# Kernel optimization log

Hardware: AMD Instinct MI355X
Metric: run time of the kernel (lower is better)

The kernel has to match this reference:

```python
import jax, jax.numpy as jnp
import numpy as np

E, K = 32, 8              # num_experts, top_k
H, I = 2048, 768          # hidden_size, moe_intermediate_size
B, S = 1, 1024            # batch, seq_len


def setup_inputs() -> dict:
    key = jax.random.key(0)
    k0, k1, k2, k3, k4 = jax.random.split(key, 5)
    scale = 0.02
    return {
        "hidden_states": jax.random.normal(k0, (B, S, H), jnp.float32),
        "gate_w":        jax.random.normal(k1, (E, H), jnp.float32) * scale,   # router, nn.Linear(H->E) weight
        "gate_proj_w":   jax.random.normal(k2, (E, I, H), jnp.float32) * scale,
        "up_proj_w":     jax.random.normal(k3, (E, I, H), jnp.float32) * scale,
        "down_proj_w":   jax.random.normal(k4, (E, H, I), jnp.float32) * scale,
    }


def reference(hidden_states, gate_w, gate_proj_w, up_proj_w, down_proj_w):
    b, s, h = hidden_states.shape
    flat = hidden_states.reshape(-1, h)                     # [T, H]
    T = flat.shape[0]

    # router
    router_logits = flat @ gate_w.T                          # [T, E]
    probs = jax.nn.softmax(router_logits.astype(jnp.float32), axis=-1)
    top_w, top_i = jax.lax.top_k(probs, K)                   # [T, K]
    top_w = top_w / jnp.sum(top_w, axis=-1, keepdims=True)   # norm_topk_prob=True
    top_w = top_w.astype(flat.dtype)

    # dense combine weights: zero for unselected experts -> same math as
    # the per-expert gather/scatter loop in the torch reference
    combine = jnp.zeros((T, E), flat.dtype).at[
        jnp.arange(T)[:, None], top_i].add(top_w)            # [T, E]

    # SwiGLU expert MLPs, batched over experts
    g = jnp.einsum('th,eih->eti', flat, gate_proj_w)         # [E, T, I]
    u = jnp.einsum('th,eih->eti', flat, up_proj_w)           # [E, T, I]
    act = jax.nn.silu(g) * u                                 # [E, T, I]
    out_e = jnp.einsum('eti,ehi->eth', act, down_proj_w)     # [E, T, H]

    final = jnp.einsum('eth,te->th', out_e, combine)         # [T, H]
    return final.reshape(b, s, h), router_logits
```

## Files before the change

### kernel.cpp

```cpp
#include <hip/hip_runtime.h>

typedef __attribute__((ext_vector_type(8))) short short8;
typedef __attribute__((ext_vector_type(8))) unsigned short ushort8;
typedef __attribute__((ext_vector_type(4))) float floatx4;

#define T_TOK 1024
#define H_DIM 2048
#define I_DIM 768
#define E_NUM 32
#define TOPK  8

#define OFF_CNT   0
#define OFF_OFFS  512
#define OFF_LIST  1024
#define OFF_TIDX  132096
#define OFF_TPOS  164864
#define OFF_TW    197632
#define OFF_ACT   262144
#define OFF_XG    12845056
#define OFF_Y     OFF_XG

__device__ __forceinline__ unsigned short f2bf(float f) {
  unsigned int u = __builtin_bit_cast(unsigned int, f);
  u += 0x7fffu + ((u >> 16) & 1u);
  return (unsigned short)(u >> 16);
}
__device__ __forceinline__ float bf2f(unsigned short h) {
  unsigned int u = ((unsigned int)h) << 16;
  return __builtin_bit_cast(float, u);
}
__device__ __forceinline__ void async_copy16(const void* g, void* l) {
  __builtin_amdgcn_global_load_lds(
      (const __attribute__((address_space(1))) unsigned int*)g,
      (__attribute__((address_space(3))) unsigned int*)l, 16, 0, 0);
}

__global__ __launch_bounds__(256) void router_kernel(
    const float* __restrict__ x, const float* __restrict__ gw,
    float* __restrict__ logits_out, int* __restrict__ cnt, int* __restrict__ list,
    int* __restrict__ tidx, int* __restrict__ tpos, float* __restrict__ tw)
{
  int t = blockIdx.x;
  int tid = threadIdx.x;
  int wave = tid >> 6, lane = tid & 63;
  const float* xr = x + (size_t)t * H_DIM;
  float xv[32];
#pragma unroll
  for (int i = 0; i < 32; i++) xv[i] = xr[lane + 64 * i];

  __shared__ float lg[E_NUM];
  for (int ee = 0; ee < 8; ee++) {
    int e = wave * 8 + ee;
    const float* wr = gw + (size_t)e * H_DIM;
    float acc = 0.f;
#pragma unroll
    for (int i = 0; i < 32; i++) acc += xv[i] * wr[lane + 64 * i];
    for (int m = 32; m >= 1; m >>= 1) acc += __shfl_xor(acc, m, 64);
    if (lane == 0) lg[e] = acc;
  }
  __syncthreads();

  if (tid < E_NUM) logits_out[t * E_NUM + tid] = lg[tid];

  if (wave == 0) {
    float logit = (lane < E_NUM) ? lg[lane] : -1e30f;
    float mx = logit;
    for (int m = 16; m >= 1; m >>= 1) mx = fmaxf(mx, __shfl_xor(mx, m, 64));
    float p = (lane < E_NUM) ? expf(logit - mx) : 0.f;
    float sum = p;
    for (int m = 16; m >= 1; m >>= 1) sum += __shfl_xor(sum, m, 64);
    p /= sum;

    float rem = (lane < E_NUM) ? p : -1.f;
    int   seli[TOPK];
    float selw[TOPK];
    float sumw = 0.f;
#pragma unroll
    for (int k = 0; k < TOPK; k++) {
      float v = rem; int i = lane;
      for (int m = 16; m >= 1; m >>= 1) {
        float ov = __shfl_xor(v, m, 64);
        int   oi = __shfl_xor(i, m, 64);
        if (ov > v || (ov == v && oi < i)) { v = ov; i = oi; }
      }
      seli[k] = i; selw[k] = v; sumw += v;
      if (lane == i) rem = -1.f;
    }
    if (lane < TOPK) {
      int e = seli[lane];
      float w = selw[lane] / sumw;
      int pos = atomicAdd(&cnt[e], 1);
      list[e * 1024 + pos] = t;
      tidx[t * TOPK + lane] = e;
      tpos[t * TOPK + lane] = pos;
      tw[t * TOPK + lane] = w;
    }
  }
}

__global__ void scan_kernel(const int* __restrict__ cnt, int* __restrict__ offs) {
  if (threadIdx.x == 0) {
    int s = 0;
    for (int e = 0; e < E_NUM; e++) { offs[e] = s; s += cnt[e]; }
    offs[E_NUM] = s;
  }
}

__global__ __launch_bounds__(256) void gather_x(
    const float* __restrict__ x, const int* __restrict__ tidx,
    const int* __restrict__ tpos, const int* __restrict__ offs,
    unsigned short* __restrict__ xg)
{
  int t = blockIdx.x;
  int tid = threadIdx.x;
  const float* xr = x + (size_t)t * H_DIM + tid * 8;
  floatx4 a = *(const floatx4*)xr;
  floatx4 b = *(const floatx4*)(xr + 4);
  ushort8 p;
#pragma unroll
  for (int j = 0; j < 4; j++) { p[j] = f2bf(a[j]); p[j + 4] = f2bf(b[j]); }
#pragma unroll
  for (int k = 0; k < TOPK; k++) {
    int e = tidx[t * TOPK + k];
    int slot = offs[e] + tpos[t * TOPK + k];
    *(ushort8*)(xg + (size_t)slot * H_DIM + tid * 8) = p;
  }
}

__global__ __launch_bounds__(256, 2) void gemm_gu(
    const unsigned short* __restrict__ xg,
    const float* __restrict__ gpw, const float* __restrict__ upw,
    const int* __restrict__ cnt, const int* __restrict__ offs,
    unsigned short* __restrict__ act)
{
  int bid = blockIdx.x;
  int e = bid & 31;
  int nt = bid >> 5;
  int c = cnt[e];
  if (c == 0) return;
  int base = offs[e];
  int n0 = nt * 32;

  __shared__ unsigned char  As[512 * 64];
  __shared__ unsigned short Ws[64 * 40];

  int tid = threadIdx.x;
  int w = tid >> 6, lane = tid & 63;
  int q = lane >> 4, l15 = lane & 15;

  int wr = tid >> 2, wc = tid & 3;
  const float* wp = (wr < 32 ? gpw + ((size_t)e * I_DIM + n0 + wr) * H_DIM
                             : upw + ((size_t)e * I_DIM + n0 + (wr - 32)) * H_DIM) + wc * 8;
  unsigned short* wdst = &Ws[wr * 40 + wc * 8];

  const unsigned short* agp[8];
  unsigned char* aldst[8];
  {
    int rl = lane >> 2;
    int ch = (lane & 3) ^ ((lane >> 3) & 3);
#pragma unroll
    for (int g = 0; g < 8; g++) {
      int rm = w * 128 + g * 16 + rl;
      int slot = base + rm; if (slot > 8191) slot = 8191;
      agp[g] = xg + (size_t)slot * H_DIM + ch * 8;
      aldst[g] = &As[(w * 128 + g * 16) * 64];
    }
  }
  const unsigned char* afp[8];
#pragma unroll
  for (int i = 0; i < 8; i++) {
    int row = w * 128 + i * 16 + l15;
    int chunk = q ^ ((row >> 1) & 3);
    afp[i] = &As[row * 64 + chunk * 16];
  }
  const unsigned short* bfp[4];
#pragma unroll
  for (int j = 0; j < 4; j++) bfp[j] = &Ws[(j * 16 + l15) * 40 + q * 8];

  int rem = c - w * 128;
  int ni = rem <= 0 ? 0 : (rem >= 128 ? 8 : ((rem + 15) >> 4));
  bool wact = ni > 0;

  floatx4 acc[8][4];
#pragma unroll
  for (int i = 0; i < 8; i++)
#pragma unroll
    for (int j = 0; j < 4; j++) acc[i][j] = (floatx4){0.f, 0.f, 0.f, 0.f};

  for (int kt = 0; kt < H_DIM / 32; kt++) {
    if (wact) {
#pragma unroll
      for (int g = 0; g < 8; g++) { async_copy16(agp[g], aldst[g]); agp[g] += 32; }
    }
    floatx4 w0 = *(const floatx4*)wp;
    floatx4 w1 = *(const floatx4*)(wp + 4);
    wp += 32;
    ushort8 pw;
#pragma unroll
    for (int z = 0; z < 4; z++) { pw[z] = f2bf(w0[z]); pw[z + 4] = f2bf(w1[z]); }
    *(ushort8*)wdst = pw;
    __syncthreads();

    short8 bf[4];
#pragma unroll
    for (int j = 0; j < 4; j++) bf[j] = *(const short8*)bfp[j];
#pragma unroll
    for (int i = 0; i < 8; i++) {
      if (i < ni) {
        short8 af = *(const short8*)afp[i];
#pragma unroll
        for (int j = 0; j < 4; j++)
          acc[i][j] = __builtin_amdgcn_mfma_f32_16x16x32_bf16(af, bf[j], acc[i][j], 0, 0, 0);
      }
    }
    __syncthreads();
  }

#pragma unroll
  for (int i = 0; i < 8; i++) {
    if (i < ni) {
#pragma unroll
      for (int r = 0; r < 4; r++) {
        int s = w * 128 + i * 16 + q * 4 + r;
        if (s < c) {
          size_t rowb = (size_t)(base + s) * I_DIM + n0;
#pragma unroll
          for (int j = 0; j < 2; j++) {
            float g = acc[i][j][r];
            float u = acc[i][j + 2][r];
            float sv = g / (1.f + __expf(-g));
            act[rowb + j * 16 + l15] = f2bf(sv * u);
          }
        }
      }
    }
  }
}

__global__ __launch_bounds__(256, 2) void gemm_down(
    const unsigned short* __restrict__ act,
    const float* __restrict__ dpw,
    const int* __restrict__ cnt, const int* __restrict__ offs,
    unsigned short* __restrict__ y)
{
  int bid = blockIdx.x;
  int e = bid & 31;
  int nt = bid >> 5;
  int c = cnt[e];
  if (c == 0) return;
  int base = offs[e];
  int h0 = nt * 64;

  __shared__ unsigned char  As[512 * 64];
  __shared__ unsigned short Ws[64 * 40];

  int tid = threadIdx.x;
  int w = tid >> 6, lane = tid & 63;
  int q = lane >> 4, l15 = lane & 15;

  int wr = tid >> 2, wc = tid & 3;
  const float* wp = dpw + ((size_t)e * H_DIM + h0 + wr) * I_DIM + wc * 8;
  unsigned short* wdst = &Ws[wr * 40 + wc * 8];

  const unsigned short* agp[8];
  unsigned char* aldst[8];
  {
    int rl = lane >> 2;
    int ch = (lane & 3) ^ ((lane >> 3) & 3);
#pragma unroll
    for (int g = 0; g < 8; g++) {
      int rm = w * 128 + g * 16 + rl;
      int slot = base + rm; if (slot > 8191) slot = 8191;
      agp[g] = act + (size_t)slot * I_DIM + ch * 8;
      aldst[g] = &As[(w * 128 + g * 16) * 64];
    }
  }
  const unsigned char* afp[8];
#pragma unroll
  for (int i = 0; i < 8; i++) {
    int row = w * 128 + i * 16 + l15;
    int chunk = q ^ ((row >> 1) & 3);
    afp[i] = &As[row * 64 + chunk * 16];
  }
  const unsigned short* bfp[4];
#pragma unroll
  for (int j = 0; j < 4; j++) bfp[j] = &Ws[(j * 16 + l15) * 40 + q * 8];

  int rem = c - w * 128;
  int ni = rem <= 0 ? 0 : (rem >= 128 ? 8 : ((rem + 15) >> 4));
  bool wact = ni > 0;

  floatx4 acc[8][4];
#pragma unroll
  for (int i = 0; i < 8; i++)
#pragma unroll
    for (int j = 0; j < 4; j++) acc[i][j] = (floatx4){0.f, 0.f, 0.f, 0.f};

  for (int kt = 0; kt < I_DIM / 32; kt++) {
    if (wact) {
#pragma unroll
      for (int g = 0; g < 8; g++) { async_copy16(agp[g], aldst[g]); agp[g] += 32; }
    }
    floatx4 w0 = *(const floatx4*)wp;
    floatx4 w1 = *(const floatx4*)(wp + 4);
    wp += 32;
    ushort8 pw;
#pragma unroll
    for (int z = 0; z < 4; z++) { pw[z] = f2bf(w0[z]); pw[z + 4] = f2bf(w1[z]); }
    *(ushort8*)wdst = pw;
    __syncthreads();

    short8 bf[4];
#pragma unroll
    for (int j = 0; j < 4; j++) bf[j] = *(const short8*)bfp[j];
#pragma unroll
    for (int i = 0; i < 8; i++) {
      if (i < ni) {
        short8 af = *(const short8*)afp[i];
#pragma unroll
        for (int j = 0; j < 4; j++)
          acc[i][j] = __builtin_amdgcn_mfma_f32_16x16x32_bf16(af, bf[j], acc[i][j], 0, 0, 0);
      }
    }
    __syncthreads();
  }

#pragma unroll
  for (int i = 0; i < 8; i++) {
    if (i < ni) {
#pragma unroll
      for (int r = 0; r < 4; r++) {
        int s = w * 128 + i * 16 + q * 4 + r;
        if (s < c) {
          size_t rowb = (size_t)(base + s) * H_DIM + h0;
#pragma unroll
          for (int j = 0; j < 4; j++)
            y[rowb + j * 16 + l15] = f2bf(acc[i][j][r]);
        }
      }
    }
  }
}

__global__ __launch_bounds__(256) void combine_kernel(
    const unsigned short* __restrict__ y,
    const int* __restrict__ tidx, const int* __restrict__ tpos,
    const float* __restrict__ tw, const int* __restrict__ offs,
    float* __restrict__ out)
{
  int t = blockIdx.x;
  int tid = threadIdx.x;
  int h = tid * 8;
  float acc[8];
#pragma unroll
  for (int j = 0; j < 8; j++) acc[j] = 0.f;
#pragma unroll
  for (int k = 0; k < TOPK; k++) {
    int e = tidx[t * TOPK + k];
    int p = tpos[t * TOPK + k];
    float w = tw[t * TOPK + k];
    size_t sg = (size_t)offs[e] + p;
    ushort8 v = *(const ushort8*)(y + sg * H_DIM + h);
#pragma unroll
    for (int j = 0; j < 8; j++) acc[j] += w * bf2f(v[j]);
  }
  floatx4 o0 = {acc[0], acc[1], acc[2], acc[3]};
  floatx4 o1 = {acc[4], acc[5], acc[6], acc[7]};
  *(floatx4*)(out + (size_t)t * H_DIM + h) = o0;
  *(floatx4*)(out + (size_t)t * H_DIM + h + 4) = o1;
}

extern "C" void kernel_launch(void* const* d_in, const int* in_sizes, int n_in,
                              void* d_out, int out_size, void* d_ws, size_t ws_size,
                              hipStream_t stream) {
  const float* x   = (const float*)d_in[0];
  const float* gw  = (const float*)d_in[1];
  const float* gpw = (const float*)d_in[2];
  const float* upw = (const float*)d_in[3];
  const float* dpw = (const float*)d_in[4];
  float* out = (float*)d_out;
  float* logits_out = out + (size_t)T_TOK * H_DIM;

  char* ws = (char*)d_ws;
  int*   cnt  = (int*)(ws + OFF_CNT);
  int*   offs = (int*)(ws + OFF_OFFS);
  int*   list = (int*)(ws + OFF_LIST);
  int*   tidx = (int*)(ws + OFF_TIDX);
  int*   tpos = (int*)(ws + OFF_TPOS);
  float* tw   = (float*)(ws + OFF_TW);
  unsigned short* act = (unsigned short*)(ws + OFF_ACT);
  unsigned short* xg  = (unsigned short*)(ws + OFF_XG);
  unsigned short* y   = (unsigned short*)(ws + OFF_Y);

  hipMemsetAsync(cnt, 0, 128, stream);
  router_kernel<<<T_TOK, 256, 0, stream>>>(x, gw, logits_out, cnt, list, tidx, tpos, tw);
  scan_kernel<<<1, 64, 0, stream>>>(cnt, offs);
  gather_x<<<T_TOK, 256, 0, stream>>>(x, tidx, tpos, offs, xg);
  gemm_gu<<<24 * E_NUM, 256, 0, stream>>>(xg, gpw, upw, cnt, offs, act);
  gemm_down<<<32 * E_NUM, 256, 0, stream>>>(act, dpw, cnt, offs, y);
  combine_kernel<<<T_TOK, 256, 0, stream>>>(y, tidx, tpos, tw, offs, out);
}
```

Measured before the change: 787.4 us.

## Double-buffer expert GEMMs and retile to 256-row M by wider-N blocks

Both expert GEMMs now double-buffer their LDS tiles and prefetch the next K-slice into registers, so global loads overlap the MFMA work and each iteration needs only one barrier. Each block now covers 256 token rows split across two M tiles instead of 512, and a wider N tile (64 gate/up columns, 128 down columns), so each A fragment feeds 8 MFMAs. The intent is to hide load latency and raise MFMA density. In exchange, LDS use grows, and experts with more than 256 tokens re-read and re-convert their fp32 weights in both M tiles.

```diff
diff --git a/kernel.cpp b/kernel.cpp
--- a/kernel.cpp
+++ b/kernel.cpp
@@ -33,6 +33,15 @@
   __builtin_amdgcn_global_load_lds(
       (const __attribute__((address_space(1))) unsigned int*)g,
       (__attribute__((address_space(3))) unsigned int*)l, 16, 0, 0);
+}
+__device__ __forceinline__ void cvt16(const floatx4& a, const floatx4& b,
+                                      const floatx4& c, const floatx4& d,
+                                      ushort8& p0, ushort8& p1) {
+#pragma unroll
+  for (int z = 0; z < 4; z++) {
+    p0[z] = f2bf(a[z]); p0[z + 4] = f2bf(b[z]);
+    p1[z] = f2bf(c[z]); p1[z + 4] = f2bf(d[z]);
+  }
 }
 
 __global__ __launch_bounds__(256) void router_kernel(
@@ -127,6 +136,7 @@
   }
 }
 
+#define GU_NT 12
 __global__ __launch_bounds__(256, 2) void gemm_gu(
     const unsigned short* __restrict__ xg,
     const float* __restrict__ gpw, const float* __restrict__ upw,
@@ -135,99 +145,122 @@
 {
   int bid = blockIdx.x;
   int e = bid & 31;
-  int nt = bid >> 5;
+  int rest = bid >> 5;
+  int nt = rest % GU_NT;
+  int mt = rest / GU_NT;
   int c = cnt[e];
-  if (c == 0) return;
-  int base = offs[e];
-  int n0 = nt * 32;
-
-  __shared__ unsigned char  As[512 * 64];
-  __shared__ unsigned short Ws[64 * 40];
+  int m0 = mt * 256;
+  if (m0 >= c) return;
+  int crem = c - m0;
+  int base = offs[e] + m0;
+  int n0 = nt * 64;
+
+  __shared__ __align__(16) unsigned char  As[2][256 * 64];
+  __shared__ __align__(16) unsigned short Ws[2][128 * 40];
 
   int tid = threadIdx.x;
   int w = tid >> 6, lane = tid & 63;
   int q = lane >> 4, l15 = lane & 15;
 
-  int wr = tid >> 2, wc = tid & 3;
-  const float* wp = (wr < 32 ? gpw + ((size_t)e * I_DIM + n0 + wr) * H_DIM
-                             : upw + ((size_t)e * I_DIM + n0 + (wr - 32)) * H_DIM) + wc * 8;
-  unsigned short* wdst = &Ws[wr * 40 + wc * 8];
-
-  const unsigned short* agp[8];
-  unsigned char* aldst[8];
+  int wr = tid >> 1, wc = tid & 1;
+  const float* wp = (wr < 64 ? gpw + ((size_t)e * I_DIM + n0 + wr) * H_DIM
+                             : upw + ((size_t)e * I_DIM + n0 + (wr - 64)) * H_DIM) + wc * 16;
+  int wofs = wr * 40 + wc * 16;
+
+  const unsigned short* agp[4];
+  int aofs[4];
   {
     int rl = lane >> 2;
     int ch = (lane & 3) ^ ((lane >> 3) & 3);
 #pragma unroll
-    for (int g = 0; g < 8; g++) {
-      int rm = w * 128 + g * 16 + rl;
+    for (int g = 0; g < 4; g++) {
+      int rm = w * 64 + g * 16 + rl;
       int slot = base + rm; if (slot > 8191) slot = 8191;
       agp[g] = xg + (size_t)slot * H_DIM + ch * 8;
-      aldst[g] = &As[(w * 128 + g * 16) * 64];
-    }
-  }
-  const unsigned char* afp[8];
-#pragma unroll
-  for (int i = 0; i < 8; i++) {
-    int row = w * 128 + i * 16 + l15;
+      aofs[g] = (w * 64 + g * 16) * 64;
+    }
+  }
+  int afo[4];
+#pragma unroll
+  for (int i = 0; i < 4; i++) {
+    int row = w * 64 + i * 16 + l15;
     int chunk = q ^ ((row >> 1) & 3);
-    afp[i] = &As[row * 64 + chunk * 16];
-  }
-  const unsigned short* bfp[4];
-#pragma unroll
-  for (int j = 0; j < 4; j++) bfp[j] = &Ws[(j * 16 + l15) * 40 + q * 8];
-
-  int rem = c - w * 128;
-  int ni = rem <= 0 ? 0 : (rem >= 128 ? 8 : ((rem + 15) >> 4));
+    afo[i] = row * 64 + chunk * 16;
+  }
+  int bfo[8];
+#pragma unroll
+  for (int j = 0; j < 8; j++) bfo[j] = (j * 16 + l15) * 40 + q * 8;
+
+  int rem = crem - w * 64;
+  int ni = rem <= 0 ? 0 : (rem >= 64 ? 4 : ((rem + 15) >> 4));
   bool wact = ni > 0;
 
-  floatx4 acc[8][4];
-#pragma unroll
-  for (int i = 0; i < 8; i++)
-#pragma unroll
-    for (int j = 0; j < 4; j++) acc[i][j] = (floatx4){0.f, 0.f, 0.f, 0.f};
-
+  floatx4 acc[4][8];
+#pragma unroll
+  for (int i = 0; i < 4; i++)
+#pragma unroll
+    for (int j = 0; j < 8; j++) acc[i][j] = (floatx4){0.f, 0.f, 0.f, 0.f};
+
+  floatx4 wv[4];
+  if (wact) {
+#pragma unroll
+    for (int g = 0; g < 4; g++) { async_copy16(agp[g], As[0] + aofs[g]); agp[g] += 32; }
+  }
+#pragma unroll
+  for (int z = 0; z < 4; z++) wv[z] = *(const floatx4*)(wp + 4 * z);
+  wp += 32;
+  {
+    ushort8 p0, p1; cvt16(wv[0], wv[1], wv[2], wv[3], p0, p1);
+    *(ushort8*)&Ws[0][wofs] = p0;
+    *(ushort8*)&Ws[0][wofs + 8] = p1;
+  }
+  __syncthreads();
+
+  int buf = 0;
   for (int kt = 0; kt < H_DIM / 32; kt++) {
-    if (wact) {
-#pragma unroll
-      for (int g = 0; g < 8; g++) { async_copy16(agp[g], aldst[g]); agp[g] += 32; }
-    }
-    floatx4 w0 = *(const floatx4*)wp;
-    floatx4 w1 = *(const floatx4*)(wp + 4);
-    wp += 32;
-    ushort8 pw;
-#pragma unroll
-    for (int z = 0; z < 4; z++) { pw[z] = f2bf(w0[z]); pw[z + 4] = f2bf(w1[z]); }
-    *(ushort8*)wdst = pw;
-    __syncthreads();
-
-    short8 bf[4];
-#pragma unroll
-    for (int j = 0; j < 4; j++) bf[j] = *(const short8*)bfp[j];
-#pragma unroll
-    for (int i = 0; i < 8; i++) {
+    bool notlast = (kt + 1 < H_DIM / 32);
+    if (notlast) {
+      if (wact) {
+#pragma unroll
+        for (int g = 0; g < 4; g++) { async_copy16(agp[g], As[buf ^ 1] + aofs[g]); agp[g] += 32; }
+      }
+#pragma unroll
+      for (int z = 0; z < 4; z++) wv[z] = *(const floatx4*)(wp + 4 * z);
+      wp += 32;
+    }
+    short8 bfr[8];
+#pragma unroll
+    for (int j = 0; j < 8; j++) bfr[j] = *(const short8*)&Ws[buf][bfo[j]];
+#pragma unroll
+    for (int i = 0; i < 4; i++) {
       if (i < ni) {
-        short8 af = *(const short8*)afp[i];
-#pragma unroll
-        for (int j = 0; j < 4; j++)
-          acc[i][j] = __builtin_amdgcn_mfma_f32_16x16x32_bf16(af, bf[j], acc[i][j], 0, 0, 0);
-      }
-    }
-    __syncthreads();
-  }
-
-#pragma unroll
-  for (int i = 0; i < 8; i++) {
+        short8 af = *(const short8*)(As[buf] + afo[i]);
+#pragma unroll
+        for (int j = 0; j < 8; j++)
+          acc[i][j] = __builtin_amdgcn_mfma_f32_16x16x32_bf16(af, bfr[j], acc[i][j], 0, 0, 0);
+      }
+    }
+    if (notlast) {
+      ushort8 p0, p1; cvt16(wv[0], wv[1], wv[2], wv[3], p0, p1);
+      *(ushort8*)&Ws[buf ^ 1][wofs] = p0;
+      *(ushort8*)&Ws[buf ^ 1][wofs + 8] = p1;
+      __syncthreads();
+    }
+    buf ^= 1;
+  }
+
+#pragma unroll
+  for (int i = 0; i < 4; i++) {
     if (i < ni) {
 #pragma unroll
       for (int r = 0; r < 4; r++) {
-        int s = w * 128 + i * 16 + q * 4 + r;
-        if (s < c) {
+        int s = w * 64 + i * 16 + q * 4 + r;
+        if (s < crem) {
           size_t rowb = (size_t)(base + s) * I_DIM + n0;
 #pragma unroll
-          for (int j = 0; j < 2; j++) {
+          for (int j = 0; j < 4; j++) {
             float g = acc[i][j][r];
-            float u = acc[i][j + 2][r];
+            float u = acc[i][j + 4][r];
             float sv = g / (1.f + __expf(-g));
             act[rowb + j * 16 + l15] = f2bf(sv * u);
           }
@@ -237,6 +270,7 @@
   }
 }
 
+#define GD_NT 16
 __global__ __launch_bounds__(256, 2) void gemm_down(
     const unsigned short* __restrict__ act,
     const float* __restrict__ dpw,
@@ -245,96 +279,119 @@
 {
   int bid = blockIdx.x;
   int e = bid & 31;
-  int nt = bid >> 5;
+  int rest = bid >> 5;
+  int nt = rest % GD_NT;
+  int mt = rest / GD_NT;
   int c = cnt[e];
-  if (c == 0) return;
-  int base = offs[e];
-  int h0 = nt * 64;
-
-  __shared__ unsigned char  As[512 * 64];
-  __shared__ unsigned short Ws[64 * 40];
+  int m0 = mt * 256;
+  if (m0 >= c) return;
+  int crem = c - m0;
+  int base = offs[e] + m0;
+  int h0 = nt * 128;
+
+  __shared__ __align__(16) unsigned char  As[2][256 * 64];
+  __shared__ __align__(16) unsigned short Ws[2][128 * 40];
 
   int tid = threadIdx.x;
   int w = tid >> 6, lane = tid & 63;
   int q = lane >> 4, l15 = lane & 15;
 
-  int wr = tid >> 2, wc = tid & 3;
-  const float* wp = dpw + ((size_t)e * H_DIM + h0 + wr) * I_DIM + wc * 8;
-  unsigned short* wdst = &Ws[wr * 40 + wc * 8];
-
-  const unsigned short* agp[8];
-  unsigned char* aldst[8];
+  int wr = tid >> 1, wc = tid & 1;
+  const float* wp = dpw + ((size_t)e * H_DIM + h0 + wr) * I_DIM + wc * 16;
+  int wofs = wr * 40 + wc * 16;
+
+  const unsigned short* agp[4];
+  int aofs[4];
   {
     int rl = lane >> 2;
     int ch = (lane & 3) ^ ((lane >> 3) & 3);
 #pragma unroll
-    for (int g = 0; g < 8; g++) {
-      int rm = w * 128 + g * 16 + rl;
+    for (int g = 0; g < 4; g++) {
+      int rm = w * 64 + g * 16 + rl;
       int slot = base + rm; if (slot > 8191) slot = 8191;
       agp[g] = act + (size_t)slot * I_DIM + ch * 8;
-      aldst[g] = &As[(w * 128 + g * 16) * 64];
-    }
-  }
-  const unsigned char* afp[8];
-#pragma unroll
-  for (int i = 0; i < 8; i++) {
-    int row = w * 128 + i * 16 + l15;
+      aofs[g] = (w * 64 + g * 16) * 64;
+    }
+  }
+  int afo[4];
+#pragma unroll
+  for (int i = 0; i < 4; i++) {
+    int row = w * 64 + i * 16 + l15;
     int chunk = q ^ ((row >> 1) & 3);
-    afp[i] = &As[row * 64 + chunk * 16];
-  }
-  const unsigned short* bfp[4];
-#pragma unroll
-  for (int j = 0; j < 4; j++) bfp[j] = &Ws[(j * 16 + l15) * 40 + q * 8];
-
-  int rem = c - w * 128;
-  int ni = rem <= 0 ? 0 : (rem >= 128 ? 8 : ((rem + 15) >> 4));
+    afo[i] = row * 64 + chunk * 16;
+  }
+  int bfo[8];
+#pragma unroll
+  for (int j = 0; j < 8; j++) bfo[j] = (j * 16 + l15) * 40 + q * 8;
+
+  int rem = crem - w * 64;
+  int ni = rem <= 0 ? 0 : (rem >= 64 ? 4 : ((rem + 15) >> 4));
   bool wact = ni > 0;
 
-  floatx4 acc[8][4];
-#pragma unroll
-  for (int i = 0; i < 8; i++)
-#pragma unroll
-    for (int j = 0; j < 4; j++) acc[i][j] = (floatx4){0.f, 0.f, 0.f, 0.f};
-
+  floatx4 acc[4][8];
+#pragma unroll
+  for (int i = 0; i < 4; i++)
+#pragma unroll
+    for (int j = 0; j < 8; j++) acc[i][j] = (floatx4){0.f, 0.f, 0.f, 0.f};
+
+  floatx4 wv[4];
+  if (wact) {
+#pragma unroll
+    for (int g = 0; g < 4; g++) { async_copy16(agp[g], As[0] + aofs[g]); agp[g] += 32; }
+  }
+#pragma unroll
+  for (int z = 0; z < 4; z++) wv[z] = *(const floatx4*)(wp + 4 * z);
+  wp += 32;
+  {
+    ushort8 p0, p1; cvt16(wv[0], wv[1], wv[2], wv[3], p0, p1);
+    *(ushort8*)&Ws[0][wofs] = p0;
+    *(ushort8*)&Ws[0][wofs + 8] = p1;
+  }
+  __syncthreads();
+
+  int buf = 0;
   for (int kt = 0; kt < I_DIM / 32; kt++) {
-    if (wact) {
-#pragma unroll
-      for (int g = 0; g < 8; g++) { async_copy16(agp[g], aldst[g]); agp[g] += 32; }
-    }
-    floatx4 w0 = *(const floatx4*)wp;
-    floatx4 w1 = *(const floatx4*)(wp + 4);
-    wp += 32;
-    ushort8 pw;
-#pragma unroll
-    for (int z = 0; z < 4; z++) { pw[z] = f2bf(w0[z]); pw[z + 4] = f2bf(w1[z]); }
-    *(ushort8*)wdst = pw;
-    __syncthreads();
-
-    short8 bf[4];
-#pragma unroll
-    for (int j = 0; j < 4; j++) bf[j] = *(const short8*)bfp[j];
-#pragma unroll
-    for (int i = 0; i < 8; i++) {
+    bool notlast = (kt + 1 < I_DIM / 32);
+    if (notlast) {
+      if (wact) {
+#pragma unroll
+        for (int g = 0; g < 4; g++) { async_copy16(agp[g], As[buf ^ 1] + aofs[g]); agp[g] += 32; }
+      }
+#pragma unroll
+      for (int z = 0; z < 4; z++) wv[z] = *(const floatx4*)(wp + 4 * z);
+      wp += 32;
+    }
+    short8 bfr[8];
+#pragma unroll
+    for (int j = 0; j < 8; j++) bfr[j] = *(const short8*)&Ws[buf][bfo[j]];
+#pragma unroll
+    for (int i = 0; i < 4; i++) {
       if (i < ni) {
-        short8 af = *(const short8*)afp[i];
-#pragma unroll
-        for (int j = 0; j < 4; j++)
-          acc[i][j] = __builtin_amdgcn_mfma_f32_16x16x32_bf16(af, bf[j], acc[i][j], 0, 0, 0);
-      }
-    }
-    __syncthreads();
-  }
-
-#pragma unroll
-  for (int i = 0; i < 8; i++) {
+        short8 af = *(const short8*)(As[buf] + afo[i]);
+#pragma unroll
+        for (int j = 0; j < 8; j++)
+          acc[i][j] = __builtin_amdgcn_mfma_f32_16x16x32_bf16(af, bfr[j], acc[i][j], 0, 0, 0);
+      }
+    }
+    if (notlast) {
+      ushort8 p0, p1; cvt16(wv[0], wv[1], wv[2], wv[3], p0, p1);
+      *(ushort8*)&Ws[buf ^ 1][wofs] = p0;
+      *(ushort8*)&Ws[buf ^ 1][wofs + 8] = p1;
+      __syncthreads();
+    }
+    buf ^= 1;
+  }
+
+#pragma unroll
+  for (int i = 0; i < 4; i++) {
     if (i < ni) {
 #pragma unroll
       for (int r = 0; r < 4; r++) {
-        int s = w * 128 + i * 16 + q * 4 + r;
-        if (s < c) {
+        int s = w * 64 + i * 16 + q * 4 + r;
+        if (s < crem) {
           size_t rowb = (size_t)(base + s) * H_DIM + h0;
 #pragma unroll
-          for (int j = 0; j < 4; j++)
+          for (int j = 0; j < 8; j++)
             y[rowb + j * 16 + l15] = f2bf(acc[i][j][r]);
         }
       }
@@ -396,7 +453,7 @@
   router_kernel<<<T_TOK, 256, 0, stream>>>(x, gw, logits_out, cnt, list, tidx, tpos, tw);
   scan_kernel<<<1, 64, 0, stream>>>(cnt, offs);
   gather_x<<<T_TOK, 256, 0, stream>>>(x, tidx, tpos, offs, xg);
-  gemm_gu<<<24 * E_NUM, 256, 0, stream>>>(xg, gpw, upw, cnt, offs, act);
-  gemm_down<<<32 * E_NUM, 256, 0, stream>>>(act, dpw, cnt, offs, y);
+  gemm_gu<<<GU_NT * 2 * E_NUM, 256, 0, stream>>>(xg, gpw, upw, cnt, offs, act);
+  gemm_down<<<GD_NT * 2 * E_NUM, 256, 0, stream>>>(act, dpw, cnt, offs, y);
   combine_kernel<<<T_TOK, 256, 0, stream>>>(y, tidx, tpos, tw, offs, out);
 }
```

Result: faster. 709.5 us (-9.9%).
